# Kernel optimization log

Hardware: AMD Instinct MI355X
Metric: run time of the kernel (lower is better)

## Reference

```python
import jax, jax.numpy as jnp
import numpy as np

# Dimensions inferred from the module (few-shot reweighted YOLOv2 region loss)
B, C, NA, NCPA = 64, 20, 5, 1          # batch, base classes, anchors, classes-per-anchor
H, W = 19, 19                           # feature map (608 input / stride 32)
T = 50                                  # cfg.max_boxes
THRESH = 0.6
COORD_SCALE = 1.0
CLASS_SCALE = 1.0
NB = B * C                              # per-class 'image' rows, as in the torch code
A4 = NA * H * W
EPS = 1e-12
BCE_EPS = 1e-7
ANCHORS = [[1.3221, 1.73145], [3.19275, 4.00944], [5.05587, 8.09892], [9.47112, 4.84053], [11.2364, 10.0071]]


def iou_xywh(x1, y1, w1, h1, x2, y2, w2, h2):
    # center-size IoU, matches darknet bbox_iou(x1y1x2y2=False)
    l = jnp.maximum(x1 - w1 * 0.5, x2 - w2 * 0.5)
    r = jnp.minimum(x1 + w1 * 0.5, x2 + w2 * 0.5)
    t = jnp.maximum(y1 - h1 * 0.5, y2 - h2 * 0.5)
    b = jnp.minimum(y1 + h1 * 0.5, y2 + h2 * 0.5)
    inter = jnp.clip(r - l, 0.0) * jnp.clip(b - t, 0.0)
    union = w1 * h1 + w2 * h2 - inter
    return inter / jnp.maximum(union, EPS)


def setup_inputs() -> dict:
    key = jax.random.key(0)
    k1, k2, k3, k4 = jax.random.split(key, 4)
    output = jax.random.normal(k1, (NB, NA * (5 + NCPA), H, W), jnp.float32) * 0.5
    # target rows: [cls, x, y, w, h] * T, coords in (0,1); x kept > 0 so all boxes are 'valid'
    cls_ids = jax.random.randint(k2, (B, C, T), 0, C).astype(jnp.float32)
    xy = jax.random.uniform(k3, (B, C, T, 2), minval=0.05, maxval=0.95)
    wh = jax.random.uniform(k4, (B, C, T, 2), minval=0.05, maxval=0.5)
    target = jnp.concatenate([cls_ids[..., None], xy, wh], axis=-1).reshape(B, C, T * 5)
    anchors = jnp.asarray(ANCHORS, jnp.float32)
    return {"output": output, "target": target, "anchors": anchors}


def _forward(output, target, anchors):
    target = jax.lax.stop_gradient(target)
    anchors = jax.lax.stop_gradient(anchors)
    out5 = output.reshape(NB, NA, 5 + NCPA, H, W)
    x = jax.nn.sigmoid(out5[:, :, 0])
    y = jax.nn.sigmoid(out5[:, :, 1])
    w = out5[:, :, 2]
    h = out5[:, :, 3]
    conf = jax.nn.sigmoid(out5[:, :, 4])
    # class logits regrouped to original batch: (B*NA*H*W, C)
    cls = out5[:, :, 5:5 + NCPA].reshape(NB, NA, H, W)
    cls_logits = cls.reshape(B, C, NA * H * W).transpose(0, 2, 1).reshape(-1, C)
    # decode pred boxes (detached, mirroring torch's use of .data)
    grid_x = jnp.arange(W, dtype=jnp.float32)[None, None, None, :]
    grid_y = jnp.arange(H, dtype=jnp.float32)[None, None, :, None]
    aw = anchors[:, 0][None, :, None, None]
    ah = anchors[:, 1][None, :, None, None]
    px = jax.lax.stop_gradient(x) + grid_x
    py = jax.lax.stop_gradient(y) + grid_y
    pw = jnp.exp(jax.lax.stop_gradient(w)) * aw
    ph = jnp.exp(jax.lax.stop_gradient(h)) * ah
    # ground-truth boxes per row
    tgt = target.reshape(NB, T, 5)
    cls_t = tgt[:, :, 0]
    gx = tgt[:, :, 1] * W
    gy = tgt[:, :, 2] * H
    gw = tgt[:, :, 3] * W
    gh = tgt[:, :, 4] * H
    # 'break on first zero x' semantics
    valid = jnp.cumprod((tgt[:, :, 1] != 0).astype(jnp.int32), axis=1) > 0
    # stage 1: zero conf_mask where any gt IoU > thresh (scan over T to avoid (NB,T,A4) blowup)
    pxf = px.reshape(NB, A4); pyf = py.reshape(NB, A4)
    pwf = pw.reshape(NB, A4); phf = ph.reshape(NB, A4)

    def iou_step(ci, xs):
        gxt, gyt, gwt, ght, vt = xs
        iou = iou_xywh(pxf, pyf, pwf, phf, gxt[:, None], gyt[:, None], gwt[:, None], ght[:, None])
        return jnp.maximum(ci, jnp.where(vt[:, None], iou, 0.0)), None

    cur_ious, _ = jax.lax.scan(iou_step, jnp.zeros((NB, A4), jnp.float32), (gx.T, gy.T, gw.T, gh.T, valid.T))
    conf_mask0 = jnp.where(cur_ious.reshape(NB, NA, H, W) > THRESH, 0.0, 1.0)
    # best anchor per gt by wh-only IoU
    inter = jnp.minimum(gw[..., None], anchors[:, 0]) * jnp.minimum(gh[..., None], anchors[:, 1])
    union = gw[..., None] * gh[..., None] + anchors[:, 0] * anchors[:, 1] - inter
    best_n = jnp.argmax(inter / jnp.maximum(union, EPS), axis=-1).astype(jnp.int32)  # (NB,T)
    gi = gx.astype(jnp.int32)
    gj = gy.astype(jnp.int32)
    # stage 2: ordered scatter of targets (later boxes overwrite earlier, as in the torch loops)
    binds = jnp.arange(NB)
    z = jnp.zeros((NB, NA, H, W), jnp.float32)
    # seen < 12800 branch: tx=ty=0.5, tw=th=0, coord_mask=1
    carry0 = (jnp.ones_like(z), z, conf_mask0, jnp.full_like(z, 0.5), jnp.full_like(z, 0.5), z, z, z, z)

    def tgt_step(carry, xs):
        cm, clm, cfm, tx, ty, tw, th, tconf, tcls = carry
        gxt, gyt, gwt, ght, bn, git, gjt, vt, ct = xs
        idx = (binds, bn, gjt, git)

        def upd(arr, val):
            return arr.at[idx].set(jnp.where(vt, val, arr[idx]))

        aw_b = anchors[bn, 0]
        ah_b = anchors[bn, 1]
        iou = iou_xywh(gxt, gyt, gwt, ght, px[idx], py[idx], pw[idx], ph[idx])
        cm = upd(cm, 1.0)
        clm = upd(clm, 1.0)
        cfm = upd(cfm, 1.0)
        tx = upd(tx, gxt - git.astype(jnp.float32))
        ty = upd(ty, gyt - gjt.astype(jnp.float32))
        tw = upd(tw, jnp.log(jnp.maximum(gwt, EPS) / aw_b))
        th = upd(th, jnp.log(jnp.maximum(ght, EPS) / ah_b))
        tconf = upd(tconf, iou)
        tcls = upd(tcls, ct)
        return (cm, clm, cfm, tx, ty, tw, th, tconf, tcls), None

    xs = (gx.T, gy.T, gw.T, gh.T, best_n.T, gi.T, gj.T, valid.T, cls_t.T)
    (coord_mask, cls_mask, conf_mask, tx, ty, tw, th, tconf, tcls), _ = jax.lax.scan(tgt_step, carry0, xs)
    # regroup per-class rows back to original batch (neg_ratio='full' -> counts[i] == C)
    cm_grp = cls_mask.reshape(B, C, NA, H, W).sum(axis=1)
    tcls_grp = tcls.reshape(B, C, NA, H, W).sum(axis=1)
    sel = (cm_grp == 1.0).reshape(-1)           # exclude colliding cells
    labels = tcls_grp.reshape(-1).astype(jnp.int32)

    def bce_mean(p, t):
        p = jnp.clip(p, BCE_EPS, 1.0 - BCE_EPS)
        return jnp.mean(-(t * jnp.log(p) + (1.0 - t) * jnp.log(1.0 - p)))

    loss_x = COORD_SCALE * bce_mean(x * coord_mask, tx * coord_mask)
    loss_y = COORD_SCALE * bce_mean(y * coord_mask, ty * coord_mask)
    loss_w = COORD_SCALE * 0.5 * jnp.mean((w * coord_mask - tw * coord_mask) ** 2)
    loss_h = COORD_SCALE * 0.5 * jnp.mean((h * coord_mask - th * coord_mask) ** 2)
    loss_conf = 0.5 * jnp.mean((conf * conf_mask - tconf * conf_mask) ** 2)
    logp = jax.nn.log_softmax(cls_logits, axis=-1)
    nll = -jnp.take_along_axis(logp, labels[:, None], axis=1)[:, 0]
    nsel = jnp.maximum(jnp.sum(sel.astype(jnp.float32)), 1.0)
    loss_cls = CLASS_SCALE * jnp.sum(jnp.where(sel, nll, 0.0)) / nsel
    return loss_x + loss_y + loss_w + loss_h + loss_conf + loss_cls


def reference(output, target, anchors):
    return _forward(output, target, anchors)
```

## Files before the change

kernel.cpp:

```cpp
#include <hip/hip_runtime.h>
#include <math.h>

constexpr int cB   = 64;
constexpr int cC   = 20;
constexpr int cNA  = 5;
constexpr int cH   = 19;
constexpr int cW   = 19;
constexpr int cT   = 50;
constexpr int cNB  = cB * cC;
constexpr int cHW  = cH * cW;
constexpr int cA4  = cNA * cHW;
constexpr int cCH  = cNA * 6;
constexpr long cNTOT = (long)cNB * cA4;
constexpr int cCLS_BLOCKS = cB * cNA;

__device__ __constant__ float cAW[cNA]   = {1.3221f, 3.19275f, 5.05587f, 9.47112f, 11.2364f};
__device__ __constant__ float cAH[cNA]   = {1.73145f, 4.00944f, 8.09892f, 4.84053f, 10.0071f};
__device__ __constant__ float cAREA[cNA] = {2.28930345f, 12.80114796f, 40.94706183f, 45.84455262f, 112.44377644f};
__device__ __constant__ float cLNAW[cNA] = {0.27920469f, 1.16088088f, 1.62060702f, 2.24822684f, 2.41915174f};
__device__ __constant__ float cLNAH[cNA] = {0.54896100f, 1.38865236f, 2.09173157f, 1.57701337f, 2.30329495f};

constexpr int ACC_BANKS = 64;
constexpr size_t OFF_CNT = 2560;
constexpr size_t OFF_ROW = 4096;
constexpr size_t ZERO_BYTES = OFF_ROW + (size_t)cB * cA4 * 4;

__device__ __forceinline__ float fexp(float x) {
    return __builtin_amdgcn_exp2f(x * 1.4426950408889634f);
}
__device__ __forceinline__ float flog(float x) {
    return __builtin_amdgcn_logf(x) * 0.6931471805599453f;
}
__device__ __forceinline__ float frcp(float x) { return __builtin_amdgcn_rcpf(x); }
__device__ __forceinline__ float fsigmoid(float x) { return frcp(1.0f + fexp(-x)); }

typedef _Float16 h2 __attribute__((ext_vector_type(2)));
union HU { unsigned u; h2 h; };
__device__ __forceinline__ unsigned splat2(float v) {
    HU x; _Float16 f = (_Float16)v; x.h[0] = f; x.h[1] = f; return x.u;
}
constexpr float cS = 1.2649110640673518f;

__launch_bounds__(256)
__global__ void k_main(const float* __restrict__ outp, const float* __restrict__ target,
                       int* __restrict__ rowenc, double* __restrict__ acc) {
    __shared__ int s_win[cA4];
    __shared__ int s_tc[cT];
    __shared__ __align__(16) unsigned s_box[cT][8];
    __shared__ float s_tval[cT][6];
    __shared__ double s_red[3][4];
    const int tid  = threadIdx.x;
    const int nb   = blockIdx.x >> 1;
    const int half = blockIdx.x & 1;
    const int base = (half << 10) + tid;
    const int b_   = nb / cC;
    const int c_   = nb - b_ * cC;
    const float* obase = outp + (size_t)nb * (cCH * cHW);

    for (int k = tid; k < cA4; k += 256) s_win[k] = -1;
    __syncthreads();

    if (tid < 64) {
        const int t = tid;
        float xr = 1.f, yr = 0.f, wr = 0.f, hr = 0.f;
        if (t < cT) {
            const float* tg = target + (size_t)nb * (cT * 5) + t * 5;
            xr = tg[1]; yr = tg[2]; wr = tg[3]; hr = tg[4];
        }
        unsigned long long nz = __ballot(xr != 0.0f);
        if (t < cT) {
            unsigned long long below = (2ull << t) - 1ull;
            bool valid = ((~nz) & below) == 0ull;
            float gx = xr * (float)cW, gy = yr * (float)cH;
            float gw = wr * (float)cW, gh = hr * (float)cH;
            if (valid) {
                s_box[t][0] = splat2(cS * (gx - 0.5f * gw));
                s_box[t][1] = splat2(cS * (gx + 0.5f * gw));
                s_box[t][2] = splat2(cS * (gy - 0.5f * gh));
                s_box[t][3] = splat2(cS * (gy + 0.5f * gh));
                s_box[t][4] = splat2(-0.6f * (gw * gh));
                float garea = gw * gh;
                float best = -1.0f; int bn = 0;
                for (int n = 0; n < cNA; ++n) {
                    float inter = fminf(gw, cAW[n]) * fminf(gh, cAH[n]);
                    float uni   = garea + cAREA[n] - inter;
                    float r = inter / fmaxf(uni, 1e-12f);
                    if (r > best) { best = r; bn = n; }
                }
                int gi = (int)gx, gj = (int)gy;
                int cell = bn * cHW + gj * cW + gi;
                s_tc[t] = cell;
                atomicMax(&s_win[cell], t);
                const float* ob = obase + (size_t)(bn * 6) * cHW + gj * cW + gi;
                float xl = ob[0], yl = ob[cHW], wl = ob[2*cHW], hl = ob[3*cHW];
                float pxc = fsigmoid(xl) + (float)gi;
                float pyc = fsigmoid(yl) + (float)gj;
                float pw = fexp(wl) * cAW[bn], ph = fexp(hl) * cAH[bn];
                float il = fmaxf(pxc - 0.5f*pw, gx - 0.5f*gw);
                float ir = fminf(pxc + 0.5f*pw, gx + 0.5f*gw);
                float it = fmaxf(pyc - 0.5f*ph, gy - 0.5f*gh);
                float ib = fminf(pyc + 0.5f*ph, gy + 0.5f*gh);
                float inter2 = fmaxf(ir - il, 0.0f) * fmaxf(ib - it, 0.0f);
                float uni2   = pw * ph + gw * gh - inter2;
                s_tval[t][0] = gx - (float)gi;
                s_tval[t][1] = gy - (float)gj;
                s_tval[t][2] = flog(fmaxf(gw, 1e-12f)) - cLNAW[bn];
                s_tval[t][3] = flog(fmaxf(gh, 1e-12f)) - cLNAH[bn];
                s_tval[t][4] = inter2 * frcp(fmaxf(uni2, 1e-12f));
            } else {
                s_box[t][0] = splat2(1e4f);  s_box[t][1] = splat2(-1e4f);
                s_box[t][2] = splat2(1e4f);  s_box[t][3] = splat2(-1e4f);
                s_box[t][4] = splat2(0.0f);
                s_tc[t] = -1;
            }
        }
    }
    __syncthreads();
    if (half == 0 && tid < cT) {
        int cell = s_tc[tid];
        if (cell >= 0 && s_win[cell] == tid)
            atomicAdd(&rowenc[b_ * cA4 + cell], (1 << 10) | (c_ * cT + tid));
    }

    h2 pl2[2], pr2[2], pt2[2], pb2[2], ov2[2], pa06h[2];
    float conf[4], tcf[4];
    unsigned wbits = 0;
    float bce = 0.0f, sq = 0.0f;
    const h2 z2 = { (_Float16)0.0f, (_Float16)0.0f };
    constexpr float cLN2 = 0.6931471805599453f;

    #pragma unroll
    for (int u = 0; u < 4; ++u) {
        int cell = base + (u << 8);
        bool a_  = cell < cA4;
        int cc   = a_ ? cell : (cA4 - 1);
        int na   = cc / cHW;
        int rem  = cc - na * cHW;
        int j    = rem / cW;
        int i    = rem - j * cW;
        const float* ob = obase + (size_t)(na * 6) * cHW + rem;
        float xl = ob[0], yl = ob[cHW], wl = ob[2*cHW], hl = ob[3*cHW], cl = ob[4*cHW];
        float Ex = __builtin_amdgcn_exp2f(-1.4426950408889634f * xl);
        float Sx = 1.0f + Ex;
        float x  = frcp(Sx);
        float Lx = __builtin_amdgcn_logf(Sx);
        float Ey = __builtin_amdgcn_exp2f(-1.4426950408889634f * yl);
        float Sy = 1.0f + Ey;
        float y  = frcp(Sy);
        float Ly = __builtin_amdgcn_logf(Sy);
        float cf = frcp(1.0f + fexp(-cl));
        float aw = cAW[na], ah = cAH[na];
        float px = x + (float)i, py = y + (float)j;
        float pw = fexp(wl) * aw, ph = fexp(hl) * ah;
        float l0 = px - 0.5f*pw, r0 = px + 0.5f*pw;
        float t0 = py - 0.5f*ph, b0 = py + 0.5f*ph;
        float pa = pw * ph;
        int p = u >> 1, s = u & 1;
        pl2[p][s] = (_Float16)(cS * l0);  pr2[p][s] = (_Float16)(cS * r0);
        pt2[p][s] = (_Float16)(cS * t0);  pb2[p][s] = (_Float16)(cS * b0);
        pa06h[p][s] = (_Float16)(0.6f * pa);
        ov2[p][s] = (_Float16)0.0f;
        conf[u] = cf;

        float tx = 0.5f, ty = 0.5f, tw = 0.0f, th = 0.0f, tc = 0.0f;
        int wt = s_win[cc];
        bool wfl = (wt >= 0) && a_;
        if (wfl) {
            wbits |= (1u << u);
            tx = s_tval[wt][0]; ty = s_tval[wt][1];
            tw = s_tval[wt][2]; th = s_tval[wt][3];
            tc = s_tval[wt][4];
        }
        tcf[u] = tc;
        if (a_) {
            bce += (1.0f - tx) * xl + cLN2 * Lx;
            bce += (1.0f - ty) * yl + cLN2 * Ly;
            float dw = wl - tw, dh = hl - th;
            sq += dw*dw + dh*dh;
        }
    }

    #pragma unroll 10
    for (int t = 0; t < cT; ++t) {
        uint4 bx = *(const uint4*)&s_box[t][0];
        unsigned gv = s_box[t][4];
        HU a, b, c, d, e;
        a.u = bx.x; b.u = bx.y; c.u = bx.z; d.u = bx.w; e.u = gv;
        #pragma unroll
        for (int p = 0; p < 2; ++p) {
            h2 iw = __builtin_elementwise_min(pr2[p], b.h) - __builtin_elementwise_max(pl2[p], a.h);
            h2 ih = __builtin_elementwise_min(pb2[p], d.h) - __builtin_elementwise_max(pt2[p], c.h);
            iw = __builtin_elementwise_max(iw, z2);
            ov2[p] = __builtin_elementwise_max(ov2[p], iw * ih + e.h);
        }
    }

    float sc = 0.0f;
    #pragma unroll
    for (int u = 0; u < 4; ++u) {
        int cell = base + (u << 8);
        if (cell >= cA4) continue;
        int p = u >> 1, s = u & 1;
        bool wfl  = (wbits >> u) & 1;
        bool over = ov2[p][s] > pa06h[p][s];
        float cm  = wfl ? 1.0f : (over ? 0.0f : 1.0f);
        float d   = (conf[u] - tcf[u]) * cm;
        sc += d * d;
    }

    double v0 = (double)bce, v1 = (double)sq, v2 = (double)sc;
    for (int off = 32; off > 0; off >>= 1) {
        v0 += __shfl_down(v0, off);
        v1 += __shfl_down(v1, off);
        v2 += __shfl_down(v2, off);
    }
    int lane = tid & 63, wid = tid >> 6;
    if (lane == 0) { s_red[0][wid] = v0; s_red[1][wid] = v1; s_red[2][wid] = v2; }
    __syncthreads();
    if (tid == 0) {
        double a0 = s_red[0][0] + s_red[0][1] + s_red[0][2] + s_red[0][3];
        double a1 = s_red[1][0] + s_red[1][1] + s_red[1][2] + s_red[1][3];
        double a2 = s_red[2][0] + s_red[2][1] + s_red[2][2] + s_red[2][3];
        int bank = blockIdx.x & (ACC_BANKS - 1);
        atomicAdd(&acc[0*ACC_BANKS + bank], a0);
        atomicAdd(&acc[1*ACC_BANKS + bank], a1);
        atomicAdd(&acc[2*ACC_BANKS + bank], a2);
    }
}

__launch_bounds__(384)
__global__ void k_cls(const float* __restrict__ outp, const float* __restrict__ target,
                      const int* __restrict__ rowenc, double* __restrict__ acc,
                      int* __restrict__ cnt, float* __restrict__ out) {
    __shared__ double s_red[2][6];
    __shared__ int s_last;
    const int tid = threadIdx.x;
    const int b   = blockIdx.x / cNA;
    const int na  = blockIdx.x - b * cNA;
    double nll = 0.0, ns = 0.0;
    if (tid < cHW) {
        const int rem = tid;
        const float* ob = outp + ((size_t)(b * cC) * cCH + na * 6 + 5) * cHW + rem;
        float l[cC]; float m = -1e30f;
        #pragma unroll
        for (int c = 0; c < cC; ++c) {
            l[c] = ob[(size_t)c * (cCH * cHW)];
            m = fmaxf(m, l[c]);
        }
        float s = 0.0f;
        #pragma unroll
        for (int c = 0; c < cC; ++c) s += fexp(l[c] - m);
        float lse = m + flog(s);
        int row = b * cA4 + na * cHW + rem;
        int v = rowenc[row];
        if ((v >> 10) == 1) {
            int payload = v & 1023;
            int selc = payload / cT;
            int selt = payload - selc * cT;
            int label = (int)target[((size_t)(b * cC + selc) * cT + selt) * 5];
            nll = (double)(lse - l[label]);
            ns  = 1.0;
        }
    }
    for (int off = 32; off > 0; off >>= 1) {
        nll += __shfl_down(nll, off);
        ns  += __shfl_down(ns, off);
    }
    int lane = tid & 63, wid = tid >> 6;
    if (lane == 0) { s_red[0][wid] = nll; s_red[1][wid] = ns; }
    __syncthreads();
    if (tid == 0) {
        double a0 = 0.0, a1 = 0.0;
        #pragma unroll
        for (int w = 0; w < 6; ++w) { a0 += s_red[0][w]; a1 += s_red[1][w]; }
        int bank = blockIdx.x & (ACC_BANKS - 1);
        atomicAdd(&acc[3*ACC_BANKS + bank], a0);
        atomicAdd(&acc[4*ACC_BANKS + bank], a1);
        __threadfence();
        s_last = (atomicAdd(cnt, 1) == cCLS_BLOCKS - 1);
    }
    __syncthreads();
    if (s_last && tid < 64) {
        __threadfence();
        double s[5];
        #pragma unroll
        for (int j = 0; j < 5; ++j) {
            double v = atomicAdd(&acc[j * ACC_BANKS + tid], 0.0);
            for (int off = 32; off > 0; off >>= 1) v += __shfl_down(v, off);
            s[j] = v;
        }
        if (tid == 0) {
            double Ninv = 1.0 / (double)cNTOT;
            double loss = s[0] * Ninv
                        + 0.5 * s[1] * Ninv
                        + 0.5 * s[2] * Ninv
                        + s[3] / fmax(s[4], 1.0);
            out[0] = (float)loss;
        }
    }
}

extern "C" void kernel_launch(void* const* d_in, const int* in_sizes, int n_in,
                              void* d_out, int out_size, void* d_ws, size_t ws_size,
                              hipStream_t stream) {
    const float* output = (const float*)d_in[0];
    const float* target = (const float*)d_in[1];
    char* ws = (char*)d_ws;
    double* acc    = (double*)ws;
    int*    cnt    = (int*)(ws + OFF_CNT);
    int*    rowenc = (int*)(ws + OFF_ROW);

    hipMemsetAsync(ws, 0, ZERO_BYTES, stream);

    k_main<<<cNB * 2, 256, 0, stream>>>(output, target, rowenc, acc);
    k_cls<<<cCLS_BLOCKS, 384, 0, stream>>>(output, target, rowenc, acc, cnt, (float*)d_out);
}
```

Baseline: 127.0 us.

## Precompute GT boxes in prep kernel, shrink winner table, swizzle block order

Adds a k_prep kernel that, once per image row, builds the packed fp16 GT boxes into global workspace and resolves the winning target per cell with wave shuffles before doing the rowenc atomicAdd. k_main then reads the boxes from global memory instead of building them in shared memory. It also shrinks the shared winner table to the block's 1024-cell half and computes the target values inline per winning cell instead of through a shared table. Block indices are swizzled across the grid, and a fallback path is kept for when the workspace is too small. This adds a kernel launch and global reads in the inner IoU loop in exchange for less duplicated setup and shared memory per block.

Result: slower. 131.9 us (+3.9%).

```diff
diff --git a/kernel.cpp b/kernel.cpp
--- a/kernel.cpp
+++ b/kernel.cpp
@@ -24,6 +24,9 @@
 constexpr size_t OFF_CNT = 2560;
 constexpr size_t OFF_ROW = 4096;
 constexpr size_t ZERO_BYTES = OFF_ROW + (size_t)cB * cA4 * 4;
+constexpr size_t OFF_GB4 = 466432;
+constexpr size_t OFF_GB1 = OFF_GB4 + (size_t)cNB * cT * 16;
+constexpr size_t WS_NEEDED = OFF_GB1 + (size_t)cNB * cT * 4;
 
 __device__ __forceinline__ float fexp(float x) {
     return __builtin_amdgcn_exp2f(x * 1.4426950408889634f);
@@ -42,22 +45,83 @@
 constexpr float cS = 1.2649110640673518f;
 
 __launch_bounds__(256)
+__global__ void k_prep(const float* __restrict__ target, int* __restrict__ rowenc,
+                       uint4* __restrict__ gb4, unsigned* __restrict__ gb1) {
+    const int nb = blockIdx.x * 4 + (threadIdx.x >> 6);
+    const int t  = threadIdx.x & 63;
+    const int b_ = nb / cC;
+    const int c_ = nb - b_ * cC;
+
+    float xr = 1.f, yr = 0.f, wr = 0.f, hr = 0.f;
+    const bool isT = (t < cT);
+    if (isT) {
+        const float* tg = target + (size_t)nb * (cT * 5) + t * 5;
+        xr = tg[1]; yr = tg[2]; wr = tg[3]; hr = tg[4];
+    }
+    unsigned long long nz = __ballot(xr != 0.0f);
+    bool valid = false;
+    int cellv = -2 - t;
+    if (isT) {
+        unsigned long long below = (2ull << t) - 1ull;
+        valid = ((~nz) & below) == 0ull;
+        const int idx = nb * cT + t;
+        float gx = xr * (float)cW, gy = yr * (float)cH;
+        float gw = wr * (float)cW, gh = hr * (float)cH;
+        uint4 bx;
+        if (valid) {
+            bx.x = splat2(cS * (gx - 0.5f * gw));
+            bx.y = splat2(cS * (gx + 0.5f * gw));
+            bx.z = splat2(cS * (gy - 0.5f * gh));
+            bx.w = splat2(cS * (gy + 0.5f * gh));
+            gb1[idx] = splat2(-0.6f * (gw * gh));
+            float garea = gw * gh;
+            float best = -1.0f; int bn = 0;
+            for (int n = 0; n < cNA; ++n) {
+                float inter = fminf(gw, cAW[n]) * fminf(gh, cAH[n]);
+                float uni   = garea + cAREA[n] - inter;
+                float r = inter / fmaxf(uni, 1e-12f);
+                if (r > best) { best = r; bn = n; }
+            }
+            cellv = bn * cHW + (int)gy * cW + (int)gx;
+        } else {
+            bx.x = splat2(1e4f);  bx.y = splat2(-1e4f);
+            bx.z = splat2(1e4f);  bx.w = splat2(-1e4f);
+            gb1[idx] = splat2(0.0f);
+        }
+        gb4[idx] = bx;
+    }
+    bool loser = false;
+    for (int i2 = 1; i2 < cT; ++i2) {
+        int ci = __shfl(cellv, i2, 64);
+        loser |= (i2 > t) && (ci == cellv);
+    }
+    if (valid && !loser)
+        atomicAdd(&rowenc[b_ * cA4 + cellv], (1 << 10) | (c_ * cT + t));
+}
+
+template<bool GB>
+__launch_bounds__(256)
 __global__ void k_main(const float* __restrict__ outp, const float* __restrict__ target,
+                       const uint4* __restrict__ gb4, const unsigned* __restrict__ gb1,
                        int* __restrict__ rowenc, double* __restrict__ acc) {
-    __shared__ int s_win[cA4];
+    __shared__ int s_win[1024];
+    __shared__ float4 s_gt[cT];
     __shared__ int s_tc[cT];
     __shared__ __align__(16) unsigned s_box[cT][8];
-    __shared__ float s_tval[cT][6];
     __shared__ double s_red[3][4];
     const int tid  = threadIdx.x;
-    const int nb   = blockIdx.x >> 1;
-    const int half = blockIdx.x & 1;
-    const int base = (half << 10) + tid;
+    const int swz  = ((int)(blockIdx.x & 7)) * 320 + ((int)blockIdx.x >> 3);
+    const int nb   = swz >> 1;
+    const int half = swz & 1;
+    const int winoff = half << 10;
+    const int base = winoff + tid;
     const int b_   = nb / cC;
     const int c_   = nb - b_ * cC;
     const float* obase = outp + (size_t)nb * (cCH * cHW);
-
-    for (int k = tid; k < cA4; k += 256) s_win[k] = -1;
+    const int nbT = nb * cT;
+
+    s_win[tid] = -1; s_win[tid + 256] = -1;
+    s_win[tid + 512] = -1; s_win[tid + 768] = -1;
     __syncthreads();
 
     if (tid < 64) {
@@ -73,12 +137,8 @@
             bool valid = ((~nz) & below) == 0ull;
             float gx = xr * (float)cW, gy = yr * (float)cH;
             float gw = wr * (float)cW, gh = hr * (float)cH;
+            s_gt[t] = make_float4(gx, gy, gw, gh);
             if (valid) {
-                s_box[t][0] = splat2(cS * (gx - 0.5f * gw));
-                s_box[t][1] = splat2(cS * (gx + 0.5f * gw));
-                s_box[t][2] = splat2(cS * (gy - 0.5f * gh));
-                s_box[t][3] = splat2(cS * (gy + 0.5f * gh));
-                s_box[t][4] = splat2(-0.6f * (gw * gh));
                 float garea = gw * gh;
                 float best = -1.0f; int bn = 0;
                 for (int n = 0; n < cNA; ++n) {
@@ -87,39 +147,32 @@
                     float r = inter / fmaxf(uni, 1e-12f);
                     if (r > best) { best = r; bn = n; }
                 }
-                int gi = (int)gx, gj = (int)gy;
-                int cell = bn * cHW + gj * cW + gi;
-                s_tc[t] = cell;
-                atomicMax(&s_win[cell], t);
-                const float* ob = obase + (size_t)(bn * 6) * cHW + gj * cW + gi;
-                float xl = ob[0], yl = ob[cHW], wl = ob[2*cHW], hl = ob[3*cHW];
-                float pxc = fsigmoid(xl) + (float)gi;
-                float pyc = fsigmoid(yl) + (float)gj;
-                float pw = fexp(wl) * cAW[bn], ph = fexp(hl) * cAH[bn];
-                float il = fmaxf(pxc - 0.5f*pw, gx - 0.5f*gw);
-                float ir = fminf(pxc + 0.5f*pw, gx + 0.5f*gw);
-                float it = fmaxf(pyc - 0.5f*ph, gy - 0.5f*gh);
-                float ib = fminf(pyc + 0.5f*ph, gy + 0.5f*gh);
-                float inter2 = fmaxf(ir - il, 0.0f) * fmaxf(ib - it, 0.0f);
-                float uni2   = pw * ph + gw * gh - inter2;
-                s_tval[t][0] = gx - (float)gi;
-                s_tval[t][1] = gy - (float)gj;
-                s_tval[t][2] = flog(fmaxf(gw, 1e-12f)) - cLNAW[bn];
-                s_tval[t][3] = flog(fmaxf(gh, 1e-12f)) - cLNAH[bn];
-                s_tval[t][4] = inter2 * frcp(fmaxf(uni2, 1e-12f));
-            } else {
+                int cell = bn * cHW + (int)gy * cW + (int)gx;
+                if constexpr (!GB) {
+                    s_tc[t] = cell;
+                    s_box[t][0] = splat2(cS * (gx - 0.5f * gw));
+                    s_box[t][1] = splat2(cS * (gx + 0.5f * gw));
+                    s_box[t][2] = splat2(cS * (gy - 0.5f * gh));
+                    s_box[t][3] = splat2(cS * (gy + 0.5f * gh));
+                    s_box[t][4] = splat2(-0.6f * garea);
+                }
+                if (cell >= winoff && cell < winoff + 1024)
+                    atomicMax(&s_win[cell - winoff], t);
+            } else if constexpr (!GB) {
+                s_tc[t] = -1;
                 s_box[t][0] = splat2(1e4f);  s_box[t][1] = splat2(-1e4f);
                 s_box[t][2] = splat2(1e4f);  s_box[t][3] = splat2(-1e4f);
                 s_box[t][4] = splat2(0.0f);
-                s_tc[t] = -1;
             }
         }
     }
     __syncthreads();
-    if (half == 0 && tid < cT) {
-        int cell = s_tc[tid];
-        if (cell >= 0 && s_win[cell] == tid)
-            atomicAdd(&rowenc[b_ * cA4 + cell], (1 << 10) | (c_ * cT + tid));
+    if constexpr (!GB) {
+        if (tid < cT) {
+            int cell = s_tc[tid];
+            if (cell >= winoff && cell < winoff + 1024 && s_win[cell - winoff] == tid)
+                atomicAdd(&rowenc[b_ * cA4 + cell], (1 << 10) | (c_ * cT + tid));
+        }
     }
 
     h2 pl2[2], pr2[2], pt2[2], pb2[2], ov2[2], pa06h[2];
@@ -149,9 +202,8 @@
         float y  = frcp(Sy);
         float Ly = __builtin_amdgcn_logf(Sy);
         float cf = frcp(1.0f + fexp(-cl));
-        float aw = cAW[na], ah = cAH[na];
         float px = x + (float)i, py = y + (float)j;
-        float pw = fexp(wl) * aw, ph = fexp(hl) * ah;
+        float pw = fexp(wl) * cAW[na], ph = fexp(hl) * cAH[na];
         float l0 = px - 0.5f*pw, r0 = px + 0.5f*pw;
         float t0 = py - 0.5f*ph, b0 = py + 0.5f*ph;
         float pa = pw * ph;
@@ -163,13 +215,20 @@
         conf[u] = cf;
 
         float tx = 0.5f, ty = 0.5f, tw = 0.0f, th = 0.0f, tc = 0.0f;
-        int wt = s_win[cc];
+        int wt = s_win[cc - winoff];
         bool wfl = (wt >= 0) && a_;
         if (wfl) {
             wbits |= (1u << u);
-            tx = s_tval[wt][0]; ty = s_tval[wt][1];
-            tw = s_tval[wt][2]; th = s_tval[wt][3];
-            tc = s_tval[wt][4];
+            float4 g = s_gt[wt];
+            tx = g.x - (float)i;  ty = g.y - (float)j;
+            tw = flog(fmaxf(g.z, 1e-12f)) - cLNAW[na];
+            th = flog(fmaxf(g.w, 1e-12f)) - cLNAH[na];
+            float iw = fminf(r0, g.x + 0.5f*g.z) - fmaxf(l0, g.x - 0.5f*g.z);
+            float ih = fminf(b0, g.y + 0.5f*g.w) - fmaxf(t0, g.y - 0.5f*g.w);
+            iw = fmaxf(iw, 0.0f); ih = fmaxf(ih, 0.0f);
+            float inter = iw * ih;
+            float uni   = g.z * g.w + pa - inter;
+            tc = inter * frcp(fmaxf(uni, 1e-12f));
         }
         tcf[u] = tc;
         if (a_) {
@@ -182,10 +241,18 @@
 
     #pragma unroll 10
     for (int t = 0; t < cT; ++t) {
-        uint4 bx = *(const uint4*)&s_box[t][0];
-        unsigned gv = s_box[t][4];
+        unsigned w0, w1, w2, w3, w4;
+        if constexpr (GB) {
+            uint4 bx = gb4[nbT + t];
+            w0 = bx.x; w1 = bx.y; w2 = bx.z; w3 = bx.w;
+            w4 = gb1[nbT + t];
+        } else {
+            uint4 bx = *(const uint4*)&s_box[t][0];
+            w0 = bx.x; w1 = bx.y; w2 = bx.z; w3 = bx.w;
+            w4 = s_box[t][4];
+        }
         HU a, b, c, d, e;
-        a.u = bx.x; b.u = bx.y; c.u = bx.z; d.u = bx.w; e.u = gv;
+        a.u = w0; b.u = w1; c.u = w2; d.u = w3; e.u = w4;
         #pragma unroll
         for (int p = 0; p < 2; ++p) {
             h2 iw = __builtin_elementwise_min(pr2[p], b.h) - __builtin_elementwise_max(pl2[p], a.h);
@@ -306,12 +373,19 @@
     const float* output = (const float*)d_in[0];
     const float* target = (const float*)d_in[1];
     char* ws = (char*)d_ws;
-    double* acc    = (double*)ws;
-    int*    cnt    = (int*)(ws + OFF_CNT);
-    int*    rowenc = (int*)(ws + OFF_ROW);
+    double*   acc    = (double*)ws;
+    int*      cnt    = (int*)(ws + OFF_CNT);
+    int*      rowenc = (int*)(ws + OFF_ROW);
+    uint4*    gb4    = (uint4*)(ws + OFF_GB4);
+    unsigned* gb1    = (unsigned*)(ws + OFF_GB1);
 
     hipMemsetAsync(ws, 0, ZERO_BYTES, stream);
 
-    k_main<<<cNB * 2, 256, 0, stream>>>(output, target, rowenc, acc);
+    if (ws_size >= WS_NEEDED) {
+        k_prep<<<cNB / 4, 256, 0, stream>>>(target, rowenc, gb4, gb1);
+        k_main<true><<<cNB * 2, 256, 0, stream>>>(output, target, gb4, gb1, rowenc, acc);
+    } else {
+        k_main<false><<<cNB * 2, 256, 0, stream>>>(output, target, gb4, gb1, rowenc, acc);
+    }
     k_cls<<<cCLS_BLOCKS, 384, 0, stream>>>(output, target, rowenc, acc, cnt, (float*)d_out);
 }
```
